# Kernel tuning notes

Hardware: AMD Instinct MI355X
Metric: run time of the kernel (lower is better)

## Reference

```python
import jax, jax.numpy as jnp
import jax.lax as lax
import numpy as np
import math

B, T_FRAMES, H, W = 32, 8, 14, 14
C, CA = 768, 384
L = H * W + 1


def setup_inputs() -> dict:
    key = jax.random.key(0)
    ks = jax.random.split(key, 7)
    s = 0.02
    return {
        "x": jax.random.normal(ks[0], (B * T_FRAMES, L, C), dtype=jnp.float32),
        "W1": jax.random.normal(ks[1], (CA, C), dtype=jnp.float32) * s,
        "b1": jnp.zeros((CA,), dtype=jnp.float32),
        "conv_w": jax.random.normal(ks[2], (CA, 1, 3, 3, 3), dtype=jnp.float32) * s,
        "conv_b": jnp.zeros((CA,), dtype=jnp.float32),
        "W2": jax.random.normal(ks[3], (C, CA), dtype=jnp.float32) * s,
        "b2": jnp.zeros((C,), dtype=jnp.float32),
        "T": T_FRAMES,
    }


def reference(x, W1, b1, conv_w, conv_b, W2, b2, T):
    BT, Lx, Cx = x.shape
    Bb = BT // T
    Ca = W1.shape[0]
    Hh = Ww = int(round(math.sqrt(Lx - 1)))
    # fc1 on all tokens except CLS: [BT, L-1, Ca]
    h = jnp.einsum("blc,ac->bla", x[:, 1:, :], W1) + b1
    # -> [B, Ca, T, H, W] for depthwise 3d conv (groups = Ca)
    h = h.reshape(Bb, T, Hh, Ww, Ca).transpose(0, 4, 1, 2, 3)
    h = lax.conv_general_dilated(
        h, conv_w,
        window_strides=(1, 1, 1),
        padding=[(1, 1), (1, 1), (1, 1)],
        dimension_numbers=("NCDHW", "OIDHW", "NCDHW"),
        feature_group_count=Ca,
    ) + conv_b[None, :, None, None, None]
    # back to [BT, L-1, Ca]
    h = h.transpose(0, 2, 3, 4, 1).reshape(BT, Lx - 1, Ca)
    # fc2: [BT, L-1, C]
    h = jnp.einsum("bla,ca->blc", h, W2) + b2
    # residual add onto non-CLS tokens
    return x.at[:, 1:, :].add(h)
```

## Files before the change

kernel.cpp:

```cpp
#include <hip/hip_runtime.h>
#include <hip/hip_bf16.h>
#include <stdint.h>

#define BTOT   256
#define LX     197
#define CDIM   768
#define CADIM  384
#define TFR    8
#define LM1    196
#define MTOT   50176

typedef unsigned short u16;
typedef short          bf16x8 __attribute__((ext_vector_type(8)));
typedef unsigned short u16x4  __attribute__((ext_vector_type(4)));
typedef unsigned short u16x8  __attribute__((ext_vector_type(8)));
typedef float          f32x4  __attribute__((ext_vector_type(4)));

typedef const __attribute__((address_space(1))) void gvoid_t;
typedef __attribute__((address_space(3))) void       svoid_t;

static __device__ __forceinline__ u16 f2bf(float f) {
  union { float f; uint32_t u; } v; v.f = f;
  uint32_t u = v.u;
  return (u16)((u + 0x7FFFu + ((u >> 16) & 1u)) >> 16);
}
static __device__ __forceinline__ float bf2f(u16 h) {
  union { uint32_t u; float f; } v; v.u = ((uint32_t)h) << 16;
  return v.f;
}
static __device__ __forceinline__ u16 f2bf_hw(float f) {
  union { __hip_bfloat16 b; u16 u; } v;
  v.b = __float2bfloat16(f);
  return v.u;
}

__global__ void prep_small(const float4* __restrict__ x4, float4* __restrict__ out4,
                           const float* __restrict__ W1, const float* __restrict__ W2,
                           const float* __restrict__ cw, u16* __restrict__ w1b,
                           u16* __restrict__ w2b, float* __restrict__ cwT) {
  int i = blockIdx.x * blockDim.x + threadIdx.x;
  if (i < CADIM * CDIM) { w1b[i] = f2bf(W1[i]); w2b[i] = f2bf(W2[i]); }
  if (i < CADIM * 27) {
    int a = i / 27; int tap = i - a * 27;
    cwT[tap * CADIM + a] = cw[i];
  }
  if (i < BTOT * 192) {
    int f = i / 192, v = i - f * 192;
    size_t off = (size_t)f * (LX * CDIM / 4) + v;
    out4[off] = x4[off];
  }
}


__global__ __launch_bounds__(768, 2) void fc1_gemm(
    const float* __restrict__ X,
    const u16* __restrict__ Bw,
    const float* __restrict__ bias,
    u16* __restrict__ Hout)
{
  __shared__ __align__(16) u16 As[2 * 128 * 32];
  __shared__ __align__(16) u16 Bs[2 * 384 * 32];
  const int tid  = threadIdx.x;
  const int lane = tid & 63;
  const int wave = tid >> 6;
  const int m0 = blockIdx.x * 128;
  const int lm = lane & 15;
  const int lk = lane >> 4;
  const int wr = wave / 6;
  const int wc = wave - wr * 6;
  const int wm = wr * 64;
  const int wn = wc * 64;
  const bool is_a = (wave < 4);

  const int g = tid >> 3;
  const int q = tid & 7;
  size_t arow[4];
  int awst[4];
  if (is_a) {
#pragma unroll
    for (int s = 0; s < 4; ++s) {
      int row = g + 32 * s;
      int tok = m0 + row;
      int bt = tok / LM1;
      int l  = tok - bt * LM1;
      arow[s] = (size_t)(bt * LX + 1 + l) * CDIM + q * 4;
      int R    = row >> 1;
      int uu   = (row & 1) * 4 + (q >> 1);
      int slot = uu ^ (R & 7);
      awst[s]  = R * 64 + slot * 8 + (q & 1) * 4;
    }
  }

  const int wb  = wave - 4;
  const int u   = (lane & 7) ^ (lane >> 3);
  const int rr  = 2 * (lane >> 3) + (u >> 2);
  const int cko = (u & 3) * 8;
  size_t boff[3];
  int ldst[3];
  if (!is_a) {
#pragma unroll
    for (int s = 0; s < 3; ++s) {
      int row = wb * 48 + s * 16 + rr;
      boff[s] = (size_t)row * CDIM + cko;
      ldst[s] = (wb * 24 + s * 8) * 64;
    }
  }

  const int lmh   = lm >> 1;
  const int slotp = (((lm & 1) << 2) | lk) ^ lmh;
  const int abase = ((wm >> 1) + lmh) * 64 + slotp * 8;
  const int bbase = ((wn >> 1) + lmh) * 64 + slotp * 8;

  f32x4 acc[4][4];
#pragma unroll
  for (int i = 0; i < 4; i++)
#pragma unroll
    for (int j = 0; j < 4; j++) acc[i][j] = (f32x4)0.0f;

  float4 areg[4];

  if (is_a) {
#pragma unroll
    for (int s = 0; s < 4; ++s) areg[s] = *(const float4*)(X + arow[s]);
#pragma unroll
    for (int s = 0; s < 4; ++s) {
      u16x4 o;
      o[0] = f2bf_hw(areg[s].x); o[1] = f2bf_hw(areg[s].y);
      o[2] = f2bf_hw(areg[s].z); o[3] = f2bf_hw(areg[s].w);
      *(u16x4*)&As[awst[s]] = o;
    }
  } else {
#pragma unroll
    for (int s = 0; s < 3; ++s)
      __builtin_amdgcn_global_load_lds((gvoid_t*)(Bw + boff[s]),
          (svoid_t*)(Bs + ldst[s]), 16, 0, 0);
  }
  __syncthreads();

  int cur = 0;
  for (int kt = 0; kt < 23; ++kt) {
    const int k1 = (kt + 1) * 32;
    const int nb = cur ^ 1;
    if (is_a) {
#pragma unroll
      for (int s = 0; s < 4; ++s) areg[s] = *(const float4*)(X + arow[s] + k1);
    } else {
#pragma unroll
      for (int s = 0; s < 3; ++s)
        __builtin_amdgcn_global_load_lds((gvoid_t*)(Bw + boff[s] + k1),
            (svoid_t*)(Bs + nb * 12288 + ldst[s]), 16, 0, 0);
    }
    {
      const u16* Ab = As + cur * 4096;
      const u16* Bb = Bs + cur * 12288;
      bf16x8 af[4], bfr[4];
#pragma unroll
      for (int i = 0; i < 4; i++) af[i] = *(const bf16x8*)&Ab[abase + i * 512];
#pragma unroll
      for (int j = 0; j < 4; j++) bfr[j] = *(const bf16x8*)&Bb[bbase + j * 512];
#pragma unroll
      for (int i = 0; i < 4; i++)
#pragma unroll
        for (int j = 0; j < 4; j++)
          acc[i][j] = __builtin_amdgcn_mfma_f32_16x16x32_bf16(af[i], bfr[j], acc[i][j], 0, 0, 0);
    }
    if (is_a) {
#pragma unroll
      for (int s = 0; s < 4; ++s) {
        u16x4 o;
        o[0] = f2bf_hw(areg[s].x); o[1] = f2bf_hw(areg[s].y);
        o[2] = f2bf_hw(areg[s].z); o[3] = f2bf_hw(areg[s].w);
        *(u16x4*)&As[nb * 4096 + awst[s]] = o;
      }
    }
    __syncthreads();
    cur ^= 1;
  }
  {
    const u16* Ab = As + cur * 4096;
    const u16* Bb = Bs + cur * 12288;
    bf16x8 af[4], bfr[4];
#pragma unroll
    for (int i = 0; i < 4; i++) af[i] = *(const bf16x8*)&Ab[abase + i * 512];
#pragma unroll
    for (int j = 0; j < 4; j++) bfr[j] = *(const bf16x8*)&Bb[bbase + j * 512];
#pragma unroll
    for (int i = 0; i < 4; i++)
#pragma unroll
      for (int j = 0; j < 4; j++)
        acc[i][j] = __builtin_amdgcn_mfma_f32_16x16x32_bf16(af[i], bfr[j], acc[i][j], 0, 0, 0);
  }

#pragma unroll
  for (int i = 0; i < 4; i++) {
    int rbase = m0 + wm + i * 16 + lk * 4;
#pragma unroll
    for (int j = 0; j < 4; j++) {
      int col = wn + j * 16 + lm;
      float bv = bias[col];
#pragma unroll
      for (int r = 0; r < 4; r++)
        Hout[(rbase + r) * CADIM + col] = f2bf(acc[i][j][r] + bv);
    }
  }
}

__global__ __launch_bounds__(256) void dwconv(
    const u16* __restrict__ h1, const float* __restrict__ cwT,
    const float* __restrict__ cb, u16* __restrict__ h2)
{
  __shared__ __align__(16) u16 lin[3 * 196 * 32];
  const int tid = threadIdx.x;
  const int f   = blockIdx.x;
  const int cc  = blockIdx.y;
  const int tv  = f & 7;

  for (int i = tid; i < 3 * 196 * 4; i += 256) {
    int fd  = i / 784;
    int rem = i - fd * 784;
    int pos = rem >> 2;
    int c8  = rem & 3;
    int tt  = tv + fd - 1;
    u16x8 v = (u16x8)0;
    if (tt >= 0 && tt < TFR) {
      const u16* src = h1 + ((size_t)(f + fd - 1) * LM1 + pos) * CADIM
                          + cc * 32 + c8 * 8;
      v = *(const u16x8*)src;
    }
    *(u16x8*)&lin[(fd * 196 + pos) * 32 + c8 * 8] = v;
  }
  __syncthreads();

  const int cg    = tid & 3;
  const int pidx  = tid >> 2;
  const int cbase = cc * 32 + cg * 8;

  float bv[8];
#pragma unroll
  for (int c = 0; c < 8; ++c) bv[c] = cb[cbase + c];

  float acc[4][8];
  int hk[4], wk[4];
#pragma unroll
  for (int k = 0; k < 4; ++k) {
    int p = pidx + 64 * k;
    hk[k] = p / 14;
    wk[k] = p - hk[k] * 14;
#pragma unroll
    for (int c = 0; c < 8; ++c) acc[k][c] = bv[c];
  }

  for (int dt = 0; dt < 3; ++dt) {
#pragma unroll
    for (int j = 0; j < 9; ++j) {
      const int dh = j / 3 - 1, dw = j % 3 - 1;
      float w8[8];
      const float* wp8 = cwT + (dt * 9 + j) * CADIM + cbase;
#pragma unroll
      for (int c = 0; c < 8; ++c) w8[c] = wp8[c];
#pragma unroll
      for (int k = 0; k < 4; ++k) {
        int p = pidx + 64 * k;
        if (p >= 196) continue;
        int hh = hk[k] + dh, ww = wk[k] + dw;
        if (hh < 0 || hh >= 14 || ww < 0 || ww >= 14) continue;
        const u16x8 v = *(const u16x8*)&lin[(dt * 196 + hh * 14 + ww) * 32 + cg * 8];
#pragma unroll
        for (int c = 0; c < 8; ++c)
          acc[k][c] += bf2f((u16)v[c]) * w8[c];
      }
    }
  }

#pragma unroll
  for (int k = 0; k < 4; ++k) {
    int p = pidx + 64 * k;
    if (p < 196) {
      u16x8 o;
#pragma unroll
      for (int c = 0; c < 8; ++c) o[c] = f2bf(acc[k][c]);
      *(u16x8*)(h2 + ((size_t)f * LM1 + p) * CADIM + cbase) = o;
    }
  }
}

__global__ __launch_bounds__(256) void fc2_gemm(
    const u16* __restrict__ A,
    const u16* __restrict__ Bw,
    const float* __restrict__ bias,
    const float* __restrict__ x,
    float* __restrict__ out)
{
  __shared__ __align__(16) u16 As[2 * 128 * 32];
  __shared__ __align__(16) u16 Bs[2 * 128 * 32];
  const int tid  = threadIdx.x;
  const int lane = tid & 63;
  const int wave = tid >> 6;

  const int orig = blockIdx.x;
  const int lgc  = (orig & 7) * 294 + (orig >> 3);
  const int lmt  = lgc / 6;
  const int lnt  = lgc - lmt * 6;
  const int m0 = lmt * 128;
  const int n0 = lnt * 128;

  const int lm = lane & 15;
  const int lk = lane >> 4;
  const int wm = (wave & 1) * 64;
  const int wn = (wave >> 1) * 64;

  const int u   = (lane & 7) ^ (lane >> 3);
  const int rr  = 2 * (lane >> 3) + (u >> 2);
  const int cko = (u & 3) * 8;
  size_t aoff[2], boff[2];
  int ldst[2];
#pragma unroll
  for (int s = 0; s < 2; ++s) {
    int row = wave * 32 + s * 16 + rr;
    aoff[s] = (size_t)(m0 + row) * CADIM + cko;
    boff[s] = (size_t)(n0 + row) * CADIM + cko;
    ldst[s] = (wave * 16 + s * 8) * 64;
  }

  const int lmh   = lm >> 1;
  const int slotp = (((lm & 1) << 2) | lk) ^ lmh;
  const int abase = ((wm >> 1) + lmh) * 64 + slotp * 8;
  const int bbase = ((wn >> 1) + lmh) * 64 + slotp * 8;

  f32x4 acc[4][4];
#pragma unroll
  for (int i = 0; i < 4; i++)
#pragma unroll
    for (int j = 0; j < 4; j++) acc[i][j] = (f32x4)0.0f;

#pragma unroll
  for (int s = 0; s < 2; ++s) {
    __builtin_amdgcn_global_load_lds((gvoid_t*)(A + aoff[s]),
        (svoid_t*)(As + ldst[s]), 16, 0, 0);
    __builtin_amdgcn_global_load_lds((gvoid_t*)(Bw + boff[s]),
        (svoid_t*)(Bs + ldst[s]), 16, 0, 0);
  }
  __syncthreads();
  int cur = 0;
  for (int kt = 0; kt < 11; ++kt) {
    const int k1 = (kt + 1) * 32;
    const int nb = cur ^ 1;
#pragma unroll
    for (int s = 0; s < 2; ++s) {
      __builtin_amdgcn_global_load_lds((gvoid_t*)(A + aoff[s] + k1),
          (svoid_t*)(As + nb * 4096 + ldst[s]), 16, 0, 0);
      __builtin_amdgcn_global_load_lds((gvoid_t*)(Bw + boff[s] + k1),
          (svoid_t*)(Bs + nb * 4096 + ldst[s]), 16, 0, 0);
    }
    {
      const u16* Ab = As + cur * 4096;
      const u16* Bb = Bs + cur * 4096;
      bf16x8 af[4], bfr[4];
#pragma unroll
      for (int i = 0; i < 4; i++) af[i] = *(const bf16x8*)&Ab[abase + i * 512];
#pragma unroll
      for (int j = 0; j < 4; j++) bfr[j] = *(const bf16x8*)&Bb[bbase + j * 512];
#pragma unroll
      for (int i = 0; i < 4; i++)
#pragma unroll
        for (int j = 0; j < 4; j++)
          acc[i][j] = __builtin_amdgcn_mfma_f32_16x16x32_bf16(af[i], bfr[j], acc[i][j], 0, 0, 0);
    }
    __syncthreads();
    cur ^= 1;
  }
  {
    const u16* Ab = As + cur * 4096;
    const u16* Bb = Bs + cur * 4096;
    bf16x8 af[4], bfr[4];
#pragma unroll
    for (int i = 0; i < 4; i++) af[i] = *(const bf16x8*)&Ab[abase + i * 512];
#pragma unroll
    for (int j = 0; j < 4; j++) bfr[j] = *(const bf16x8*)&Bb[bbase + j * 512];
#pragma unroll
    for (int i = 0; i < 4; i++)
#pragma unroll
      for (int j = 0; j < 4; j++)
        acc[i][j] = __builtin_amdgcn_mfma_f32_16x16x32_bf16(af[i], bfr[j], acc[i][j], 0, 0, 0);
  }

  float bv[4];
#pragma unroll
  for (int j = 0; j < 4; j++) bv[j] = bias[n0 + wn + j * 16 + lm];
#pragma unroll
  for (int i = 0; i < 4; i++) {
    int rbase = m0 + wm + i * 16 + lk * 4;
    size_t orow[4];
#pragma unroll
    for (int r = 0; r < 4; r++) {
      int tok = rbase + r;
      int bt = tok / LM1;
      int l  = tok - bt * LM1;
      orow[r] = (size_t)(bt * LX + 1 + l) * CDIM + (n0 + wn + lm);
    }
    float xv[4][4];
#pragma unroll
    for (int r = 0; r < 4; r++)
#pragma unroll
      for (int j = 0; j < 4; j++)
        xv[r][j] = x[orow[r] + j * 16];
#pragma unroll
    for (int r = 0; r < 4; r++)
#pragma unroll
      for (int j = 0; j < 4; j++)
        out[orow[r] + j * 16] = xv[r][j] + acc[i][j][r] + bv[j];
  }
}

extern "C" void kernel_launch(void* const* d_in, const int* in_sizes, int n_in,
                              void* d_out, int out_size, void* d_ws, size_t ws_size,
                              hipStream_t stream) {
  const float* x  = (const float*)d_in[0];
  const float* W1 = (const float*)d_in[1];
  const float* b1 = (const float*)d_in[2];
  const float* cw = (const float*)d_in[3];
  const float* cb = (const float*)d_in[4];
  const float* W2 = (const float*)d_in[5];
  const float* b2 = (const float*)d_in[6];
  float* out = (float*)d_out;

  char* ws = (char*)d_ws;
  u16*   w1b = (u16*)(ws + 0);
  u16*   w2b = (u16*)(ws + 589824);
  float* cwT = (float*)(ws + 1179648);
  u16*   h1  = (u16*)(ws + 1245184);
  u16*   h2  = (u16*)(ws + 39780352);

  prep_small<<<1152, 256, 0, stream>>>((const float4*)x, (float4*)out,
                                       W1, W2, cw, w1b, w2b, cwT);
  fc1_gemm<<<MTOT / 128, 768, 0, stream>>>(x, w1b, b1, h1);
  dwconv  <<<dim3(BTOT, 12), 256, 0, stream>>>(h1, cwT, cb, h2);
  fc2_gemm<<<2352, 256, 0, stream>>>(h2, w2b, b2, x, out);
}
```

Before: 434.2 us.

## Register-tile depthwise conv as 2x2 output patches with fp32 swizzled LDS

The depthwise 3D conv kernel now stores the staged input tile in shared memory as fp32, using an XOR swizzle to avoid bank conflicts, so bf16 conversion happens once per element at load time. Each thread computes a 2x2 spatial output patch from a 4x4 input window, reusing every loaded input across up to four outputs, and keeps all 9 weights per temporal slice in registers. This cuts LDS reads and conversions per output. The cost is double the shared memory (about 75 KB per block, likely fewer resident blocks), more register pressure, and only 196 of 256 threads active in the compute phase.

```diff
diff --git a/kernel.cpp b/kernel.cpp
--- a/kernel.cpp
+++ b/kernel.cpp
@@ -209,7 +209,7 @@
     const u16* __restrict__ h1, const float* __restrict__ cwT,
     const float* __restrict__ cb, u16* __restrict__ h2)
 {
-  __shared__ __align__(16) u16 lin[3 * 196 * 32];
+  __shared__ __align__(16) float lin[3 * 196 * 32];
   const int tid = threadIdx.x;
   const int f   = blockIdx.x;
   const int cc  = blockIdx.y;
@@ -221,66 +221,89 @@
     int pos = rem >> 2;
     int c8  = rem & 3;
     int tt  = tv + fd - 1;
-    u16x8 v = (u16x8)0;
+    float vf[8];
+#pragma unroll
+    for (int c = 0; c < 8; ++c) vf[c] = 0.0f;
     if (tt >= 0 && tt < TFR) {
-      const u16* src = h1 + ((size_t)(f + fd - 1) * LM1 + pos) * CADIM
-                          + cc * 32 + c8 * 8;
-      v = *(const u16x8*)src;
-    }
-    *(u16x8*)&lin[(fd * 196 + pos) * 32 + c8 * 8] = v;
+      const u16x8 v = *(const u16x8*)(h1 + ((size_t)(f + fd - 1) * LM1 + pos) * CADIM
+                                         + cc * 32 + c8 * 8);
+#pragma unroll
+      for (int c = 0; c < 8; ++c) vf[c] = bf2f((u16)v[c]);
+    }
+    const int p7 = pos & 7;
+    const int s0 = (fd * 196 + pos) * 8;
+    f32x4 a, b;
+    a[0] = vf[0]; a[1] = vf[1]; a[2] = vf[2]; a[3] = vf[3];
+    b[0] = vf[4]; b[1] = vf[5]; b[2] = vf[6]; b[3] = vf[7];
+    *(f32x4*)&lin[(s0 + ((c8 * 2) ^ p7)) * 4]     = a;
+    *(f32x4*)&lin[(s0 + ((c8 * 2 + 1) ^ p7)) * 4] = b;
   }
   __syncthreads();
 
+  const int patch = tid >> 2;
   const int cg    = tid & 3;
-  const int pidx  = tid >> 2;
   const int cbase = cc * 32 + cg * 8;
-
-  float bv[8];
-#pragma unroll
-  for (int c = 0; c < 8; ++c) bv[c] = cb[cbase + c];
-
-  float acc[4][8];
-  int hk[4], wk[4];
-#pragma unroll
-  for (int k = 0; k < 4; ++k) {
-    int p = pidx + 64 * k;
-    hk[k] = p / 14;
-    wk[k] = p - hk[k] * 14;
-#pragma unroll
-    for (int c = 0; c < 8; ++c) acc[k][c] = bv[c];
-  }
-
-  for (int dt = 0; dt < 3; ++dt) {
-#pragma unroll
-    for (int j = 0; j < 9; ++j) {
-      const int dh = j / 3 - 1, dw = j % 3 - 1;
-      float w8[8];
-      const float* wp8 = cwT + (dt * 9 + j) * CADIM + cbase;
-#pragma unroll
-      for (int c = 0; c < 8; ++c) w8[c] = wp8[c];
-#pragma unroll
-      for (int k = 0; k < 4; ++k) {
-        int p = pidx + 64 * k;
-        if (p >= 196) continue;
-        int hh = hk[k] + dh, ww = wk[k] + dw;
-        if (hh < 0 || hh >= 14 || ww < 0 || ww >= 14) continue;
-        const u16x8 v = *(const u16x8*)&lin[(dt * 196 + hh * 14 + ww) * 32 + cg * 8];
-#pragma unroll
-        for (int c = 0; c < 8; ++c)
-          acc[k][c] += bf2f((u16)v[c]) * w8[c];
+  if (patch < 49) {
+    const int hp = patch / 7, wp = patch - hp * 7;
+    const int h0 = hp * 2, w0 = wp * 2;
+
+    float acc[2][2][8];
+#pragma unroll
+    for (int c = 0; c < 8; ++c) {
+      float bv = cb[cbase + c];
+      acc[0][0][c] = bv; acc[0][1][c] = bv; acc[1][0][c] = bv; acc[1][1][c] = bv;
+    }
+
+    for (int dt = 0; dt < 3; ++dt) {
+      float wreg[9][8];
+#pragma unroll
+      for (int j = 0; j < 9; ++j) {
+        const float* wp8 = cwT + (dt * 9 + j) * CADIM + cbase;
+#pragma unroll
+        for (int c = 0; c < 8; ++c) wreg[j][c] = wp8[c];
       }
-    }
-  }
-
-#pragma unroll
-  for (int k = 0; k < 4; ++k) {
-    int p = pidx + 64 * k;
-    if (p < 196) {
-      u16x8 o;
-#pragma unroll
-      for (int c = 0; c < 8; ++c) o[c] = f2bf(acc[k][c]);
-      *(u16x8*)(h2 + ((size_t)f * LM1 + p) * CADIM + cbase) = o;
-    }
+#pragma unroll
+      for (int ih = 0; ih < 4; ++ih) {
+        int hh = h0 - 1 + ih;
+        if (hh < 0 || hh >= 14) continue;
+#pragma unroll
+        for (int iw = 0; iw < 4; ++iw) {
+          int ww = w0 - 1 + iw;
+          if (ww < 0 || ww >= 14) continue;
+          const int pos = hh * 14 + ww;
+          const int p7  = pos & 7;
+          const int s0  = (dt * 196 + pos) * 8;
+          const f32x4 va = *(const f32x4*)&lin[(s0 + ((cg * 2) ^ p7)) * 4];
+          const f32x4 vb = *(const f32x4*)&lin[(s0 + ((cg * 2 + 1) ^ p7)) * 4];
+          float vf[8];
+          vf[0] = va[0]; vf[1] = va[1]; vf[2] = va[2]; vf[3] = va[3];
+          vf[4] = vb[0]; vf[5] = vb[1]; vf[6] = vb[2]; vf[7] = vb[3];
+#pragma unroll
+          for (int oh = 0; oh < 2; ++oh) {
+            if (ih - 1 - oh < -1 || ih - 1 - oh > 1) continue;
+#pragma unroll
+            for (int ow = 0; ow < 2; ++ow) {
+              if (iw - 1 - ow < -1 || iw - 1 - ow > 1) continue;
+              const int j = (ih - oh) * 3 + (iw - ow);
+#pragma unroll
+              for (int c = 0; c < 8; ++c)
+                acc[oh][ow][c] += vf[c] * wreg[j][c];
+            }
+          }
+        }
+      }
+    }
+
+    const size_t obase = (size_t)f * LM1 * CADIM + cbase;
+#pragma unroll
+    for (int oh = 0; oh < 2; ++oh)
+#pragma unroll
+      for (int ow = 0; ow < 2; ++ow) {
+        u16x8 o;
+#pragma unroll
+        for (int c = 0; c < 8; ++c) o[c] = f2bf(acc[oh][ow][c]);
+        *(u16x8*)(h2 + obase + ((size_t)(h0 + oh) * 14 + w0 + ow) * CADIM) = o;
+      }
   }
 }
 
```

Result: no change. 440.4 us (+1.4%).
